# Performance work log

Measured on AMD Instinct MI355X. Metric: run time of the kernel, lower is better.

## Reference

```python
import jax, jax.numpy as jnp
import numpy as np

EPS = 1e-5
NEG_SLOPE = 0.2  # DGL GATConv default leaky_relu slope


def conv1d_same(x, w, b):
    # x: [N, Cin, T], w: [Cout, Cin, K]
    y = jax.lax.conv_general_dilated(x, w, (1,), 'SAME',
                                     dimension_numbers=('NCW', 'OIW', 'NCW'))
    return y + b[None, :, None]


def gated_conv(x, w1, b1, w2, b2, w3, b3):
    # Temporal_Gated_Conv: relu(conv1(x)*sigmoid(conv2(x)) + conv3(x))
    return jax.nn.relu(conv1d_same(x, w1, b1) * jax.nn.sigmoid(conv1d_same(x, w2, b2))
                       + conv1d_same(x, w3, b3))


def bn3(x, g, b):
    # BatchNorm1d on [N, C, T]: stats over (N, T), training mode (batch stats)
    m = jnp.mean(x, (0, 2), keepdims=True)
    v = jnp.var(x, (0, 2), keepdims=True)
    return (x - m) * jax.lax.rsqrt(v + EPS) * g[None, :, None] + b[None, :, None]


def bn2(x, g, b):
    # BatchNorm1d on [N, F]: stats over N
    m = jnp.mean(x, 0, keepdims=True)
    v = jnp.var(x, 0, keepdims=True)
    return (x - m) * jax.lax.rsqrt(v + EPS) * g[None, :] + b[None, :]


def setup_inputs() -> dict:
    key = jax.random.key(0)
    ks = jax.random.split(key, 24)
    N, C, T, H, DEG = 20000, 32, 8, 4, 16
    F = C * T          # GAT in/out feats per head = 256
    E = N * DEG
    s = 0.05
    inp = {
        'X': jax.random.normal(ks[0], (N, C, T), jnp.float32),
        'src': jax.random.randint(ks[1], (E,), 0, N, jnp.int32),
        'dst': jax.random.randint(ks[2], (E,), 0, N, jnp.int32),
        # residual_proj: Conv1d(C->C, k=1)
        'rp_w': jax.random.normal(ks[3], (C, C, 1), jnp.float32) * s,
        'rp_b': jnp.zeros((C,), jnp.float32),
        # gated_conv1: three Conv1d(C->C, k=3)
        'g1_w1': jax.random.normal(ks[4], (C, C, 3), jnp.float32) * s,
        'g1_b1': jnp.zeros((C,), jnp.float32),
        'g1_w2': jax.random.normal(ks[5], (C, C, 3), jnp.float32) * s,
        'g1_b2': jnp.zeros((C,), jnp.float32),
        'g1_w3': jax.random.normal(ks[6], (C, C, 3), jnp.float32) * s,
        'g1_b3': jnp.zeros((C,), jnp.float32),
        'bn0_g': jnp.ones((C,), jnp.float32),
        'bn0_b': jnp.zeros((C,), jnp.float32),
        # GATConv: fc [H*F, F], attn_l/attn_r [H, F], bias [H*F]
        'gat_w': jax.random.normal(ks[7], (H * F, F), jnp.float32) * s,
        'attn_l': jax.random.normal(ks[8], (H, F), jnp.float32) * s,
        'attn_r': jax.random.normal(ks[9], (H, F), jnp.float32) * s,
        'gat_bias': jnp.zeros((H * F,), jnp.float32),
        'bn1_g': jnp.ones((H * F,), jnp.float32),
        'bn1_b': jnp.zeros((H * F,), jnp.float32),
        # gated_conv2: three Conv1d(C*H -> C, k=3)
        'g2_w1': jax.random.normal(ks[10], (C, C * H, 3), jnp.float32) * s,
        'g2_b1': jnp.zeros((C,), jnp.float32),
        'g2_w2': jax.random.normal(ks[11], (C, C * H, 3), jnp.float32) * s,
        'g2_b2': jnp.zeros((C,), jnp.float32),
        'g2_w3': jax.random.normal(ks[12], (C, C * H, 3), jnp.float32) * s,
        'g2_b3': jnp.zeros((C,), jnp.float32),
        'bn2_g': jnp.ones((C,), jnp.float32),
        'bn2_b': jnp.zeros((C,), jnp.float32),
    }
    return inp


def reference(X, src, dst, rp_w, rp_b, g1_w1, g1_b1, g1_w2, g1_b2, g1_w3, g1_b3,
              bn0_g, bn0_b, gat_w, attn_l, attn_r, gat_bias, bn1_g, bn1_b,
              g2_w1, g2_b1, g2_w2, g2_b2, g2_w3, g2_b3, bn2_g, bn2_b):
    N, C, T = X.shape
    H, F = attn_l.shape

    residual = conv1d_same(X, rp_w, rp_b)                      # [N, C, T]
    x = gated_conv(X, g1_w1, g1_b1, g1_w2, g1_b2, g1_w3, g1_b3)
    x = bn3(x, bn0_g, bn0_b)
    x = x.reshape(N, C * T)                                    # row-major flatten == torch .view

    # --- DGL GATConv (feat_drop=attn_drop=0, concat heads, ReLU activation) ---
    h = (x @ gat_w.T).reshape(N, H, F)                         # fc projection
    el = jnp.sum(h * attn_l, -1)                               # [N, H]
    er = jnp.sum(h * attn_r, -1)                               # [N, H]
    e = jax.nn.leaky_relu(el[src] + er[dst], NEG_SLOPE)        # [E, H]
    # segment softmax over incoming edges of each dst node
    m = jax.ops.segment_max(e, dst, num_segments=N)            # [N, H]
    ee = jnp.exp(e - m[dst])
    den = jax.ops.segment_sum(ee, dst, num_segments=N)         # [N, H]
    alpha = ee / den[dst]                                      # [E, H]
    rst = jax.ops.segment_sum(alpha[:, :, None] * h[src], dst, num_segments=N)  # [N, H, F]
    rst = jax.nn.relu(rst + gat_bias.reshape(H, F))

    x = rst.reshape(N, H * F)                                  # concat heads
    x = bn2(x, bn1_g, bn1_b)
    x = x.reshape(N, (H * F) // T, T)                          # [N, C*H, T]
    x = gated_conv(x, g2_w1, g2_b1, g2_w2, g2_b2, g2_w3, g2_b3)
    x = bn3(x, bn2_g, bn2_b)
    x = jax.nn.relu(x + residual)                              # self.last=True, dropout=0
    return x
```

## Files before the change

### kernel.cpp

```cpp
#include <hip/hip_runtime.h>
#include <stdint.h>

#define NN 20000
#define NE 320000

typedef unsigned short us16;
typedef __attribute__((ext_vector_type(8))) short short8;
typedef __attribute__((ext_vector_type(4))) float f32x4;

union U4 { uint4 v; us16 s[8]; unsigned u[4]; };
union U2 { uint2 v; us16 s[4]; };

__device__ __forceinline__ float b2f(us16 u){ return __uint_as_float(((unsigned)u)<<16); }
__device__ __forceinline__ us16 f2b(float f){
  unsigned u = __float_as_uint(f);
  u += 0x7fffu + ((u>>16)&1u);
  return (us16)(u>>16);
}

__device__ __forceinline__ void gll16(const void* g, void* l){
  __builtin_amdgcn_global_load_lds((const __attribute__((address_space(1))) void*)g,
                                   (__attribute__((address_space(3))) void*)l, 16, 0, 0);
}

__global__ __launch_bounds__(256) void k_misc(
    const float* __restrict__ gatw, us16* __restrict__ Wb,
    const float* __restrict__ w1, const float* __restrict__ w2, const float* __restrict__ w3,
    us16* __restrict__ Wt,
    const float* __restrict__ c1w1, const float* __restrict__ c1w2, const float* __restrict__ c1w3,
    const float* __restrict__ rp_w, us16* __restrict__ Wt1,
    const float* __restrict__ attnl, const float* __restrict__ attnr,
    float* __restrict__ wl, float* __restrict__ wr,
    const int* __restrict__ dst, int* __restrict__ counts)
{
  const int b = blockIdx.x, tid = threadIdx.x;
  if(b < 256){
    int i = b*256 + tid;
    float4 v = *(const float4*)(gatw + (size_t)i*4);
    U2 o;
    o.s[0]=f2b(v.x); o.s[1]=f2b(v.y); o.s[2]=f2b(v.z); o.s[3]=f2b(v.w);
    *(uint2*)(Wb + (size_t)i*4) = o.v;
  } else if(b < 400){
    int i = (b-256)*256 + tid;
    int s = i/12288, rem = i%12288;
    int co3 = rem>>7, ci = rem&127;
    const float* w = (co3<32) ? w1 : (co3<64) ? w2 : w3;
    Wt[i] = f2b(w[(co3&31)*384 + ci*3 + s]);
  } else if(b < 448){
    int i = (b-400)*256 + tid;
    int s = i>>12, rem = i&4095;
    int co3 = rem>>5, ci = rem&31;
    float v;
    if(co3 < 96){
      const float* w = (co3<32) ? c1w1 : (co3<64) ? c1w2 : c1w3;
      v = w[(co3&31)*96 + ci*3 + s];
    } else {
      v = (s==1) ? rp_w[(co3-96)*32 + ci] : 0.f;
    }
    Wt1[i] = f2b(v);
  } else if(b < 480){
    int bb = b-448;
    int sel = bb>>4, hd = (bb>>2)&3, fq = bb&3;
    const float* attn = sel ? attnr : attnl;
    int k = tid;
    float s = 0.f;
    int f0 = fq*64;
    #pragma unroll 8
    for(int f=f0; f<f0+64; f++)
      s = fmaf(attn[hd*256+f], gatw[(size_t)(hd*256+f)*256 + k], s);
    atomicAdd(&((sel ? wr : wl)[hd*256+k]), s);
  } else {
    int e = (b-480)*256 + tid;
    if(e < NE) atomicAdd(&counts[dst[e]], 1);
  }
}

__global__ __launch_bounds__(256) void k_gemm1(
    const float* __restrict__ X, const us16* __restrict__ Wt1,
    const float* __restrict__ b1, const float* __restrict__ b2, const float* __restrict__ b3,
    const float* __restrict__ rp_b,
    us16* __restrict__ gc1, us16* __restrict__ resid,
    float* __restrict__ bn0_sum, float* __restrict__ bn0_sq,
    const int* __restrict__ counts, int* __restrict__ offsets, int* __restrict__ cursor)
{
  __shared__ float smemF[5760];
  __shared__ float redS[32], redQ[32];
  __shared__ int wred[4];
  const int tid = threadIdx.x;
  if(blockIdx.x < 1250){
    us16* As = (us16*)smemF;
    us16* Bs = As + 6400;
    if(tid<32){ redS[tid]=0.f; redQ[tid]=0.f; }
    const int node0 = blockIdx.x*16;
    const int lane = tid&63, wv = tid>>6;
    const int mrow = lane&15, kg = (lane>>4)*8;
    for(int idx=tid; idx<1024; idx+=256){
      int n = idx>>6, rem = idx&63, slot = (rem>>5)*9, ci = rem&31;
      As[n*400 + slot*40 + ci] = 0;
    }
    #pragma unroll
    for(int i=0;i<4;i++){
      int idx = i*256 + tid;
      int n = idx>>6, rem = idx&63, ci = rem>>1, tq = rem&1;
      float4 xv = *(const float4*)(X + (size_t)(node0+n)*256 + ci*8 + tq*4);
      us16* p = &As[n*400 + (tq*4+1)*40 + ci];
      p[0]   = f2b(xv.x);
      p[40]  = f2b(xv.y);
      p[80]  = f2b(xv.z);
      p[120] = f2b(xv.w);
    }
    f32x4 acc[2][8] = {};
    for(int s=0; s<3; s++){
      if(s) __syncthreads();
      #pragma unroll
      for(int i=0;i<2;i++){
        int c = i*256 + tid;
        int co = c>>2, cq = c&3;
        *(uint4*)&Bs[co*40 + cq*8] = *(const uint4*)(Wt1 + s*4096 + co*32 + cq*8);
      }
      __syncthreads();
      short8 af[2], bfr[8];
      #pragma unroll
      for(int i=0;i<2;i++){
        int r = wv*32 + i*16 + mrow;
        af[i] = *(const short8*)&As[(r>>3)*400 + ((r&7)+s)*40 + kg];
      }
      #pragma unroll
      for(int j=0;j<8;j++)
        bfr[j] = *(const short8*)&Bs[(j*16 + mrow)*40 + kg];
      #pragma unroll
      for(int i=0;i<2;i++){
        #pragma unroll
        for(int j=0;j<8;j++)
          acc[i][j] = __builtin_amdgcn_mfma_f32_16x16x32_bf16(af[i], bfr[j], acc[i][j], 0, 0, 0);
      }
    }
    __syncthreads();
    us16* Og = (us16*)smemF;
    us16* Or = Og + 4096;
    const int coA = lane&15, coB = coA+16;
    const float b1A=b1[coA], b2A=b2[coA], b3A=b3[coA], brA=rp_b[coA];
    const float b1B=b1[coB], b2B=b2[coB], b3B=b3[coB], brB=rp_b[coB];
    float sA=0.f, qA=0.f, sB=0.f, qB=0.f;
    const int g = lane>>4;
    #pragma unroll
    for(int i=0;i<2;i++){
      int node = wv*4 + i*2 + (g>>1);
      int t0 = (g&1)*4;
      U2 pA, pB, rA2, rB2;
      #pragma unroll
      for(int r=0;r<4;r++){
        float c1 = acc[i][0][r]+b1A, c2 = acc[i][2][r]+b2A, c3 = acc[i][4][r]+b3A;
        float rr = acc[i][6][r]+brA;
        float sg = 1.f/(1.f+__expf(-c2));
        float v = fmaf(c1,sg,c3); v = v>0.f ? v : 0.f;
        sA += v; qA += v*v;
        pA.s[r]=f2b(v); rA2.s[r]=f2b(rr);
        c1 = acc[i][1][r]+b1B; c2 = acc[i][3][r]+b2B; c3 = acc[i][5][r]+b3B;
        rr = acc[i][7][r]+brB;
        sg = 1.f/(1.f+__expf(-c2));
        v = fmaf(c1,sg,c3); v = v>0.f ? v : 0.f;
        sB += v; qB += v*v;
        pB.s[r]=f2b(v); rB2.s[r]=f2b(rr);
      }
      *(uint2*)&Og[node*256 + coA*8 + t0] = pA.v;
      *(uint2*)&Og[node*256 + coB*8 + t0] = pB.v;
      *(uint2*)&Or[node*256 + coA*8 + t0] = rA2.v;
      *(uint2*)&Or[node*256 + coB*8 + t0] = rB2.v;
    }
    sA += __shfl_xor(sA,16,64); sA += __shfl_xor(sA,32,64);
    qA += __shfl_xor(qA,16,64); qA += __shfl_xor(qA,32,64);
    sB += __shfl_xor(sB,16,64); sB += __shfl_xor(sB,32,64);
    qB += __shfl_xor(qB,16,64); qB += __shfl_xor(qB,32,64);
    if(lane < 16){
      atomicAdd(&redS[coA], sA); atomicAdd(&redQ[coA], qA);
      atomicAdd(&redS[coB], sB); atomicAdd(&redQ[coB], qB);
    }
    __syncthreads();
    #pragma unroll
    for(int i=0;i<2;i++){
      int idx = i*256 + tid;
      *(uint4*)(gc1   + (size_t)node0*256 + (size_t)idx*8) = *(const uint4*)&Og[idx*8];
      *(uint4*)(resid + (size_t)node0*256 + (size_t)idx*8) = *(const uint4*)&Or[idx*8];
    }
    if(tid<32)      atomicAdd(&bn0_sum[tid], redS[tid]);
    else if(tid<64) atomicAdd(&bn0_sq[tid-32], redQ[tid-32]);
  } else {
    const int lane = tid&63, wv = tid>>6;
    int running = 0;
    int4 cur;
    {
      int idx = tid*4;
      cur = *(const int4*)(counts + idx);
    }
    for(int t=0; t<20; t++){
      int4 nxt; nxt.x=0; nxt.y=0; nxt.z=0; nxt.w=0;
      if(t < 19){
        int idx = (t+1)*1024 + tid*4;
        if(idx+3 < NN) nxt = *(const int4*)(counts + idx);
        else {
          if(idx   < NN) nxt.x = counts[idx];
          if(idx+1 < NN) nxt.y = counts[idx+1];
          if(idx+2 < NN) nxt.z = counts[idx+2];
          if(idx+3 < NN) nxt.w = counts[idx+3];
        }
      }
      int s = cur.x + cur.y + cur.z + cur.w;
      int incl = s;
      #pragma unroll
      for(int off=1; off<64; off<<=1){
        int v = __shfl_up(incl, off, 64);
        if(lane >= off) incl += v;
      }
      if(lane==63) wred[wv] = incl;
      __syncthreads();
      int woff = 0, btot = 0;
      #pragma unroll
      for(int w2=0; w2<4; w2++){
        int x = wred[w2];
        btot += x;
        if(w2 < wv) woff += x;
      }
      int e0 = running + woff + incl - s;
      int idx = t*1024 + tid*4;
      int4 o; o.x=e0; o.y=e0+cur.x; o.z=o.y+cur.y; o.w=o.z+cur.z;
      if(idx+3 < NN){
        *(int4*)(offsets+idx) = o;
        *(int4*)(cursor+idx)  = o;
      } else {
        if(idx   < NN){ offsets[idx]  =o.x; cursor[idx]  =o.x; }
        if(idx+1 < NN){ offsets[idx+1]=o.y; cursor[idx+1]=o.y; }
        if(idx+2 < NN){ offsets[idx+2]=o.z; cursor[idx+2]=o.z; }
        if(idx+3 < NN){ offsets[idx+3]=o.w; cursor[idx+3]=o.w; }
      }
      running += btot;
      cur = nxt;
      __syncthreads();
    }
    if(tid==0) offsets[NN] = running;
  }
}

__global__ __launch_bounds__(256) void k_eler2(const us16* __restrict__ gc1,
    const float* __restrict__ bn0_sum, const float* __restrict__ bn0_sq,
    const float* __restrict__ bn0g, const float* __restrict__ bn0b,
    const float* __restrict__ wl, const float* __restrict__ wr,
    float* __restrict__ el, float* __restrict__ er)
{
  __shared__ float sa[32], sb[32];
  const int tid = threadIdx.x;
  if(tid<32){
    float m = bn0_sum[tid]*(1.f/160000.f);
    float v = bn0_sq[tid]*(1.f/160000.f) - m*m;
    float a = bn0g[tid]*rsqrtf(v + 1e-5f);
    sa[tid] = a; sb[tid] = bn0b[tid] - m*a;
  }
  __syncthreads();
  const int wv = tid>>6, lane = tid&63;
  const int node = blockIdx.x*4 + wv;
  U2 g; g.v = *(const uint2*)(gc1 + (size_t)node*256 + lane*4);
  const float a = sa[lane>>1], b = sb[lane>>1];
  float xv[4];
  #pragma unroll
  for(int j=0;j<4;j++) xv[j] = fmaf(a, b2f(g.s[j]), b);
  float res[8];
  #pragma unroll
  for(int hd=0; hd<4; hd++){
    float4 lv = *(const float4*)(wl + hd*256 + lane*4);
    float4 rv = *(const float4*)(wr + hd*256 + lane*4);
    res[hd]   = xv[0]*lv.x + xv[1]*lv.y + xv[2]*lv.z + xv[3]*lv.w;
    res[4+hd] = xv[0]*rv.x + xv[1]*rv.y + xv[2]*rv.z + xv[3]*rv.w;
  }
  #pragma unroll
  for(int o=32;o;o>>=1){
    #pragma unroll
    for(int k=0;k<8;k++) res[k] += __shfl_xor(res[k], o, 64);
  }
  if(lane==0){
    #pragma unroll
    for(int hd=0;hd<4;hd++){ el[node*4+hd]=res[hd]; er[node*4+hd]=res[4+hd]; }
  }
}

__global__ __launch_bounds__(256) void k_scatter(const int* __restrict__ src, const int* __restrict__ dst,
    int* __restrict__ cursor, int* __restrict__ esrc,
    const float* __restrict__ el, const float* __restrict__ er,
    float* __restrict__ ew)
{
  int e = blockIdx.x*256 + threadIdx.x;
  if(e < NE){
    int s = src[e], d = dst[e];
    int pos = atomicAdd(&cursor[d], 1);
    esrc[pos] = s;
    float4 lv = *(const float4*)(el + s*4);
    float4 rv = *(const float4*)(er + d*4);
    float4 sc;
    sc.x = lv.x+rv.x; sc.x = sc.x>0.f ? sc.x : 0.2f*sc.x;
    sc.y = lv.y+rv.y; sc.y = sc.y>0.f ? sc.y : 0.2f*sc.y;
    sc.z = lv.z+rv.z; sc.z = sc.z>0.f ? sc.z : 0.2f*sc.z;
    sc.w = lv.w+rv.w; sc.w = sc.w>0.f ? sc.w : 0.2f*sc.w;
    *(float4*)(ew + (size_t)pos*4) = sc;
  }
}

__global__ __launch_bounds__(256) void k_agg2(
    const int* __restrict__ offsets, const int* __restrict__ esrc,
    const float* __restrict__ ew, const us16* __restrict__ gc1,
    const float* __restrict__ bn0_sum, const float* __restrict__ bn0_sq,
    const float* __restrict__ bn0g, const float* __restrict__ bn0b,
    us16* __restrict__ Axg)
{
  const int tid = threadIdx.x;
  const int wv = tid>>6, lane = tid&63;
  const int node = blockIdx.x*4 + wv;
  const int ch = lane>>1;
  float mmn = bn0_sum[ch]*(1.f/160000.f);
  float vvn = bn0_sq[ch]*(1.f/160000.f) - mmn*mmn;
  float sa = bn0g[ch]*rsqrtf(vvn + 1e-5f);
  float sb = bn0b[ch] - mmn*sa;
  const int beg = offsets[node];
  const int deg = offsets[node+1] - beg;
  const int h = lane>>4, i0 = lane&15;
  float m = -3.0e38f;
  for(int i=i0; i<deg; i+=16) m = fmaxf(m, ew[(size_t)(beg+i)*4 + h]);
  m = fmaxf(m, __shfl_xor(m,1,64)); m = fmaxf(m, __shfl_xor(m,2,64));
  m = fmaxf(m, __shfl_xor(m,4,64)); m = fmaxf(m, __shfl_xor(m,8,64));
  float den = 0.f;
  for(int i=i0; i<deg; i+=16) den += __expf(ew[(size_t)(beg+i)*4 + h] - m);
  den += __shfl_xor(den,1,64); den += __shfl_xor(den,2,64);
  den += __shfl_xor(den,4,64); den += __shfl_xor(den,8,64);
  const float m0=__shfl(m,0,64),   m1=__shfl(m,16,64),  m2=__shfl(m,32,64),  m3=__shfl(m,48,64);
  const float d0=__shfl(den,0,64), d1=__shfl(den,16,64),d2=__shfl(den,32,64),d3=__shfl(den,48,64);
  const float v0=d0>0.f?1.f/d0:0.f, v1=d1>0.f?1.f/d1:0.f,
              v2=d2>0.f?1.f/d2:0.f, v3=d3>0.f?1.f/d3:0.f;
  float a0c[4]={},a1c[4]={},a2c[4]={},a3c[4]={};
  #pragma unroll 4
  for(int j=0; j<deg; j++){
    int pos = beg+j;
    float4 w4 = *(const float4*)(ew + (size_t)pos*4);
    int sN = esrc[pos];
    U2 hv; hv.v = *(const uint2*)(gc1 + (size_t)sN*256 + lane*4);
    float e0 = __expf(w4.x-m0)*v0;
    float e1 = __expf(w4.y-m1)*v1;
    float e2 = __expf(w4.z-m2)*v2;
    float e3 = __expf(w4.w-m3)*v3;
    #pragma unroll
    for(int kk=0;kk<4;kk++){
      float x = b2f(hv.s[kk]);
      a0c[kk] = fmaf(e0,x,a0c[kk]);
      a1c[kk] = fmaf(e1,x,a1c[kk]);
      a2c[kk] = fmaf(e2,x,a2c[kk]);
      a3c[kk] = fmaf(e3,x,a3c[kk]);
    }
  }
  const float sbi = sb * ((deg>0)?1.f:0.f);
  U2 o0,o1,o2,o3;
  #pragma unroll
  for(int kk=0;kk<4;kk++){
    o0.s[kk]=f2b(fmaf(sa,a0c[kk],sbi));
    o1.s[kk]=f2b(fmaf(sa,a1c[kk],sbi));
    o2.s[kk]=f2b(fmaf(sa,a2c[kk],sbi));
    o3.s[kk]=f2b(fmaf(sa,a3c[kk],sbi));
  }
  *(uint2*)(Axg + ((size_t)node)*256            + lane*4) = o0.v;
  *(uint2*)(Axg + ((size_t)NN + node)*256       + lane*4) = o1.v;
  *(uint2*)(Axg + ((size_t)2*NN + node)*256     + lane*4) = o2.v;
  *(uint2*)(Axg + ((size_t)3*NN + node)*256     + lane*4) = o3.v;
}

__global__ __launch_bounds__(256) void k_gemm3(const us16* __restrict__ Axg, const us16* __restrict__ Wb,
    const float* __restrict__ gbias, us16* __restrict__ rst,
    float* __restrict__ bn1_sum, float* __restrict__ bn1_sq)
{
  __shared__ us16 sm[17408];
  us16* As = sm;
  us16* Bs = sm + 4096;
  const int tid = threadIdx.x;
  const int row0 = blockIdx.x*128;
  const int cb   = blockIdx.y*128;
  const int hd   = blockIdx.z;
  const us16* A = Axg + (size_t)hd*NN*256;
  const us16* B = Wb  + (size_t)(hd*256 + cb)*256;
  const int lane = tid&63, wv = tid>>6;
  const int wm = wv&1, wn = wv>>1;
  const int mrow = lane&15, g4 = lane>>4;
  const us16* sgA[2]; const us16* sgB[2];
  us16* sdA[2]; us16* sdB[2];
  #pragma unroll
  for(int i=0;i<2;i++){
    int r = (i*4+wv)*16 + (lane>>2);
    int c = (lane&3) ^ (r&3);
    int ga = row0 + r; if(ga >= NN) ga = NN-1;
    sgA[i] = A + (size_t)ga*256 + c*8;
    sgB[i] = B + (size_t)r*256 + c*8;
    sdA[i] = As + (i*4+wv)*512;
    sdB[i] = Bs + (i*4+wv)*512;
  }
  f32x4 acc[4][4] = {};
  for(int k0=0; k0<256; k0+=32){
    if(k0) __syncthreads();
    #pragma unroll
    for(int i=0;i<2;i++){
      gll16(sgA[i] + k0, sdA[i]);
      gll16(sgB[i] + k0, sdB[i]);
    }
    __syncthreads();
    short8 af[4], bfr[4];
    #pragma unroll
    for(int i=0;i<4;i++){
      int r = wm*64 + i*16 + mrow;
      af[i] = *(const short8*)&As[r*32 + ((g4 ^ (r&3))<<3)];
    }
    #pragma unroll
    for(int j=0;j<4;j++){
      int r = wn*64 + j*16 + mrow;
      bfr[j] = *(const short8*)&Bs[r*32 + ((g4 ^ (r&3))<<3)];
    }
    #pragma unroll
    for(int i=0;i<4;i++){
      #pragma unroll
      for(int j=0;j<4;j++)
        acc[i][j] = __builtin_amdgcn_mfma_f32_16x16x32_bf16(af[i], bfr[j], acc[i][j], 0, 0, 0);
    }
  }
  float gb[4];
  #pragma unroll
  for(int j=0;j<4;j++)
    gb[j] = gbias[hd*256 + cb + wn*64 + j*16 + (lane&15)];
  __syncthreads();
  us16* Og = sm;
  float cs[4]={}, cq[4]={};
  #pragma unroll
  for(int i=0;i<4;i++){
    #pragma unroll
    for(int j=0;j<4;j++){
      #pragma unroll
      for(int r=0;r<4;r++){
        int rl = wm*64 + i*16 + (lane>>4)*4 + r;
        float v = acc[i][j][r] + gb[j];
        v = v>0.f ? v : 0.f;
        Og[rl*136 + wn*64 + j*16 + (lane&15)] = f2b(v);
        if(row0 + rl < NN){ cs[j] += v; cq[j] += v*v; }
      }
    }
  }
  #pragma unroll
  for(int j=0;j<4;j++){
    cs[j] += __shfl_xor(cs[j],16,64); cs[j] += __shfl_xor(cs[j],32,64);
    cq[j] += __shfl_xor(cq[j],16,64); cq[j] += __shfl_xor(cq[j],32,64);
  }
  if(lane < 16){
    #pragma unroll
    for(int j=0;j<4;j++){
      int col = hd*256 + cb + wn*64 + j*16 + lane;
      atomicAdd(&bn1_sum[col], cs[j]);
      atomicAdd(&bn1_sq[col],  cq[j]);
    }
  }
  __syncthreads();
  #pragma unroll
  for(int i=0;i<8;i++){
    int idx = i*256 + tid;
    int rowl = idx>>4, cq2 = idx&15;
    int g = row0 + rowl;
    if(g < NN)
      *(uint4*)(rst + (size_t)g*1024 + hd*256 + cb + cq2*8) = *(const uint4*)&Og[rowl*136 + cq2*8];
  }
}

__global__ __launch_bounds__(256) void k_gemm2(
    const us16* __restrict__ rst, const us16* __restrict__ Wt,
    const float* __restrict__ bn1_sum, const float* __restrict__ bn1_sq,
    const float* __restrict__ bn1g, const float* __restrict__ bn1b,
    const float* __restrict__ b1, const float* __restrict__ b2, const float* __restrict__ b3,
    us16* __restrict__ y2, float* __restrict__ bn2_sum, float* __restrict__ bn2_sq)
{
  __shared__ us16 As[11520];
  __shared__ us16 Bs[6912];
  __shared__ float redS[32], redQ[32];
  const int tid = threadIdx.x;
  if(tid<32){ redS[tid]=0.f; redQ[tid]=0.f; }
  const int node0 = blockIdx.x*16;
  const int lane = tid&63, wv = tid>>6;
  const int mrow = lane&15, kg = (lane>>4)*8;
  for(int idx=tid; idx<2048; idx+=256){
    int n = idx>>7, rem = idx&127, slot = (rem>>6)*9, ci = rem&63;
    As[n*720 + slot*72 + ci] = 0;
  }
  f32x4 acc[2][6] = {};
  for(int kc=0; kc<2; kc++){
    float ra[8], rb[8];
    {
      int f0 = (kc*64 + (tid&63))*8;
      float4 s0 = *(const float4*)(bn1_sum + f0), s1 = *(const float4*)(bn1_sum + f0 + 4);
      float4 q0 = *(const float4*)(bn1_sq  + f0), q1 = *(const float4*)(bn1_sq  + f0 + 4);
      float4 g0 = *(const float4*)(bn1g    + f0), g1 = *(const float4*)(bn1g    + f0 + 4);
      float4 h0 = *(const float4*)(bn1b    + f0), h1 = *(const float4*)(bn1b    + f0 + 4);
      const float* sp = (const float*)&s0; const float* qp = (const float*)&q0;
      const float* gp = (const float*)&g0; const float* hp = (const float*)&h0;
      #pragma unroll
      for(int t=0;t<8;t++){
        float sv = (t<4)? sp[t] : ((const float*)&s1)[t-4];
        float qv = (t<4)? qp[t] : ((const float*)&q1)[t-4];
        float gv = (t<4)? gp[t] : ((const float*)&g1)[t-4];
        float hv = (t<4)? hp[t] : ((const float*)&h1)[t-4];
        float m = sv*(1.f/20000.f);
        float v = qv*(1.f/20000.f) - m*m;
        float a = gv*rsqrtf(v + 1e-5f);
        ra[t] = a; rb[t] = hv - m*a;
      }
    }
    if(kc) __syncthreads();
    #pragma unroll
    for(int i=0;i<4;i++){
      int idx = i*256 + tid;
      int n = idx>>6, cil = idx&63;
      int ci = kc*64 + cil;
      U4 in; in.v = *(const uint4*)(rst + (size_t)(node0+n)*1024 + ci*8);
      us16* p = &As[n*720 + 72 + cil];
      #pragma unroll
      for(int t=0;t<8;t++)
        p[t*72] = f2b(fmaf(ra[t], b2f(in.s[t]), rb[t]));
    }
    for(int s=0; s<3; s++){
      if(s) __syncthreads();
      #pragma unroll
      for(int i=0;i<3;i++){
        int chunk = i*256 + tid;
        int brow = chunk>>3, cc = chunk&7;
        *(uint4*)&Bs[brow*72 + cc*8] =
          *(const uint4*)(Wt + s*12288 + brow*128 + kc*64 + cc*8);
      }
      __syncthreads();
      #pragma unroll
      for(int kk=0; kk<64; kk+=32){
        short8 af[2], bfr[6];
        #pragma unroll
        for(int i=0;i<2;i++){
          int r = wv*32 + i*16 + mrow;
          af[i] = *(const short8*)&As[(r>>3)*720 + ((r&7)+s)*72 + kk + kg];
        }
        #pragma unroll
        for(int j=0;j<6;j++)
          bfr[j] = *(const short8*)&Bs[(j*16 + mrow)*72 + kk + kg];
        #pragma unroll
        for(int i=0;i<2;i++){
          #pragma unroll
          for(int j=0;j<6;j++)
            acc[i][j] = __builtin_amdgcn_mfma_f32_16x16x32_bf16(af[i], bfr[j], acc[i][j], 0, 0, 0);
        }
      }
    }
  }
  __syncthreads();
  us16* Og = (us16*)As;
  const int coA = lane&15, coB = coA+16;
  const float b1A=b1[coA], b2A=b2[coA], b3A=b3[coA];
  const float b1B=b1[coB], b2B=b2[coB], b3B=b3[coB];
  float sA=0.f, qA=0.f, sB=0.f, qB=0.f;
  const int g = lane>>4;
  #pragma unroll
  for(int i=0;i<2;i++){
    int node = wv*4 + i*2 + (g>>1);
    int t0 = (g&1)*4;
    U2 pA, pB;
    #pragma unroll
    for(int r=0;r<4;r++){
      float c1 = acc[i][0][r]+b1A, c2 = acc[i][2][r]+b2A, c3 = acc[i][4][r]+b3A;
      float sg = 1.f/(1.f+__expf(-c2));
      float v = fmaf(c1,sg,c3); v = v>0.f ? v : 0.f;
      sA += v; qA += v*v; pA.s[r]=f2b(v);
      c1 = acc[i][1][r]+b1B; c2 = acc[i][3][r]+b2B; c3 = acc[i][5][r]+b3B;
      sg = 1.f/(1.f+__expf(-c2));
      v = fmaf(c1,sg,c3); v = v>0.f ? v : 0.f;
      sB += v; qB += v*v; pB.s[r]=f2b(v);
    }
    *(uint2*)&Og[node*256 + coA*8 + t0] = pA.v;
    *(uint2*)&Og[node*256 + coB*8 + t0] = pB.v;
  }
  sA += __shfl_xor(sA,16,64); sA += __shfl_xor(sA,32,64);
  qA += __shfl_xor(qA,16,64); qA += __shfl_xor(qA,32,64);
  sB += __shfl_xor(sB,16,64); sB += __shfl_xor(sB,32,64);
  qB += __shfl_xor(qB,16,64); qB += __shfl_xor(qB,32,64);
  if(lane < 16){
    atomicAdd(&redS[coA], sA); atomicAdd(&redQ[coA], qA);
    atomicAdd(&redS[coB], sB); atomicAdd(&redQ[coB], qB);
  }
  __syncthreads();
  #pragma unroll
  for(int i=0;i<2;i++){
    int idx = i*256 + tid;
    *(uint4*)(y2 + (size_t)node0*256 + (size_t)idx*8) = *(const uint4*)&Og[idx*8];
  }
  if(tid<32)      atomicAdd(&bn2_sum[tid], redS[tid]);
  else if(tid<64) atomicAdd(&bn2_sq[tid-32], redQ[tid-32]);
}

__global__ __launch_bounds__(256) void k_final(const us16* __restrict__ y2,
    const float* __restrict__ bn2_sum, const float* __restrict__ bn2_sq,
    const float* __restrict__ bn2g, const float* __restrict__ bn2b,
    const us16* __restrict__ resid, float* __restrict__ out)
{
  __shared__ float fa[32], fb[32];
  const int tid = threadIdx.x;
  if(tid<32){
    float m = bn2_sum[tid]*(1.f/160000.f);
    float v = bn2_sq[tid]*(1.f/160000.f) - m*m;
    float a = bn2g[tid]*rsqrtf(v + 1e-5f);
    fa[tid] = a; fb[tid] = bn2b[tid] - m*a;
  }
  __syncthreads();
  size_t base = ((size_t)blockIdx.x*256 + tid)*8;
  int ch = (int)((base>>3)&31);
  float a = fa[ch], b = fb[ch];
  U4 yv, rv;
  yv.v = *(const uint4*)(y2+base);
  rv.v = *(const uint4*)(resid+base);
  float4 o0, o1;
  float vv[8];
  #pragma unroll
  for(int j=0;j<8;j++){
    float v = fmaf(a, b2f(yv.s[j]), b) + b2f(rv.s[j]);
    vv[j] = v>0.f ? v : 0.f;
  }
  o0.x=vv[0]; o0.y=vv[1]; o0.z=vv[2]; o0.w=vv[3];
  o1.x=vv[4]; o1.y=vv[5]; o1.z=vv[6]; o1.w=vv[7];
  *(float4*)(out+base)   = o0;
  *(float4*)(out+base+4) = o1;
}

extern "C" void kernel_launch(void* const* d_in, const int* in_sizes, int n_in,
                              void* d_out, int out_size, void* d_ws, size_t ws_size,
                              hipStream_t stream)
{
  const float* X    = (const float*)d_in[0];
  const int*  src   = (const int*)d_in[1];
  const int*  dst   = (const int*)d_in[2];
  const float* rp_w = (const float*)d_in[3];
  const float* rp_b = (const float*)d_in[4];
  const float* g1w1 = (const float*)d_in[5];
  const float* g1b1 = (const float*)d_in[6];
  const float* g1w2 = (const float*)d_in[7];
  const float* g1b2 = (const float*)d_in[8];
  const float* g1w3 = (const float*)d_in[9];
  const float* g1b3 = (const float*)d_in[10];
  const float* bn0g = (const float*)d_in[11];
  const float* bn0b = (const float*)d_in[12];
  const float* gatw = (const float*)d_in[13];
  const float* attnl= (const float*)d_in[14];
  const float* attnr= (const float*)d_in[15];
  const float* gbias= (const float*)d_in[16];
  const float* bn1g = (const float*)d_in[17];
  const float* bn1b = (const float*)d_in[18];
  const float* g2w1 = (const float*)d_in[19];
  const float* g2b1 = (const float*)d_in[20];
  const float* g2w2 = (const float*)d_in[21];
  const float* g2b2 = (const float*)d_in[22];
  const float* g2w3 = (const float*)d_in[23];
  const float* g2b3 = (const float*)d_in[24];
  const float* bn2g = (const float*)d_in[25];
  const float* bn2b = (const float*)d_in[26];
  float* out = (float*)d_out;
  (void)in_sizes; (void)n_in; (void)out_size; (void)ws_size;

  char* w = (char*)d_ws;
  float* bn0_sum = (float*)w;
  float* bn0_sq  = bn0_sum + 32;
  float* bn1_sum = bn0_sum + 64;
  float* bn1_sq  = bn1_sum + 1024;
  float* bn2_sum = bn1_sq  + 1024;
  float* bn2_sq  = bn2_sum + 32;
  float* wl      = bn2_sq + 32;
  float* wr      = wl + 1024;
  int*   counts  = (int*)(wr + 1024);
  size_t zeroBytes = (size_t)((char*)(counts + NN) - w);
  int*   offsets = counts + NN;
  int*   cursor  = offsets + 20004;
  int*   esrc    = cursor + NN;
  float* el      = (float*)(esrc + NE);
  float* er      = el + NN*4;
  float* ew      = er + NN*4;
  us16*  wb      = (us16*)(ew + (size_t)NE*4);
  us16*  resid   = wb + 262144;
  us16*  gc1     = resid + 5120000;
  us16*  Axg     = gc1   + 5120000;
  us16*  rst     = Axg   + 20480000;
  us16*  Wt      = rst   + 20480000;
  us16*  Wt1     = Wt    + 36864;
  us16*  y2      = gc1;

  hipMemsetAsync(d_ws, 0, zeroBytes, stream);
  k_misc<<<1730, 256, 0, stream>>>(gatw, wb, g2w1, g2w2, g2w3, Wt,
                                   g1w1, g1w2, g1w3, rp_w, Wt1,
                                   attnl, attnr, wl, wr, dst, counts);
  k_gemm1<<<1251, 256, 0, stream>>>(X, Wt1, g1b1, g1b2, g1b3, rp_b,
                                    gc1, resid, bn0_sum, bn0_sq,
                                    counts, offsets, cursor);
  k_eler2<<<5000, 256, 0, stream>>>(gc1, bn0_sum, bn0_sq, bn0g, bn0b, wl, wr, el, er);
  k_scatter<<<1250, 256, 0, stream>>>(src, dst, cursor, esrc, el, er, ew);
  k_agg2<<<5000, 256, 0, stream>>>(offsets, esrc, ew, gc1, bn0_sum, bn0_sq, bn0g, bn0b, Axg);
  k_gemm3<<<dim3(157, 2, 4), 256, 0, stream>>>(Axg, wb, gbias, rst, bn1_sum, bn1_sq);
  k_gemm2<<<1250, 256, 0, stream>>>(rst, Wt, bn1_sum, bn1_sq, bn1g, bn1b,
                                    g2b1, g2b2, g2b3, y2, bn2_sum, bn2_sq);
  k_final<<<2500, 256, 0, stream>>>(y2, bn2_sum, bn2_sq, bn2g, bn2b, resid, out);
}
```

Baseline: 340.8 us.

## Widen gemm3 block to full 256-column head tile with 512 threads

k_gemm3 now uses 512-thread blocks covering all 256 output columns of a head instead of two 128-column blocks, so each A tile row-slab is loaded from global memory once rather than twice. The epilogue is split into two passes through the shared staging buffer, since it only holds 128 columns. This halves redundant A traffic but halves the block count (628 vs 1256), adds extra syncs in the epilogue, and raises per-block resource use.

```diff
diff --git a/kernel.cpp b/kernel.cpp
--- a/kernel.cpp
+++ b/kernel.cpp
@@ -368,7 +368,7 @@
   *(uint2*)(Axg + ((size_t)3*NN + node)*256     + lane*4) = o3.v;
 }
 
-__global__ __launch_bounds__(256) void k_gemm3(const us16* __restrict__ Axg, const us16* __restrict__ Wb,
+__global__ __launch_bounds__(512) void k_gemm3(const us16* __restrict__ Axg, const us16* __restrict__ Wb,
     const float* __restrict__ gbias, us16* __restrict__ rst,
     float* __restrict__ bn1_sum, float* __restrict__ bn1_sq)
 {
@@ -377,33 +377,34 @@
   us16* Bs = sm + 4096;
   const int tid = threadIdx.x;
   const int row0 = blockIdx.x*128;
-  const int cb   = blockIdx.y*128;
-  const int hd   = blockIdx.z;
-  const us16* A = Axg + (size_t)hd*NN*256;
-  const us16* B = Wb  + (size_t)(hd*256 + cb)*256;
+  const int hd   = blockIdx.y;
+  const us16* A  = Axg + (size_t)hd*NN*256;
+  const us16* Bf = Wb  + (size_t)hd*256*256;
   const int lane = tid&63, wv = tid>>6;
   const int wm = wv&1, wn = wv>>1;
   const int mrow = lane&15, g4 = lane>>4;
-  const us16* sgA[2]; const us16* sgB[2];
-  us16* sdA[2]; us16* sdB[2];
-  #pragma unroll
-  for(int i=0;i<2;i++){
-    int r = (i*4+wv)*16 + (lane>>2);
+  const us16* sgA; const us16* sgB[2];
+  us16 *sdA, *sdB[2];
+  {
+    int r = wv*16 + (lane>>2);
     int c = (lane&3) ^ (r&3);
     int ga = row0 + r; if(ga >= NN) ga = NN-1;
-    sgA[i] = A + (size_t)ga*256 + c*8;
-    sgB[i] = B + (size_t)r*256 + c*8;
-    sdA[i] = As + (i*4+wv)*512;
-    sdB[i] = Bs + (i*4+wv)*512;
+    sgA = A + (size_t)ga*256 + c*8;
+    sdA = As + wv*512;
+    #pragma unroll
+    for(int i=0;i<2;i++){
+      int rb = wv*32 + i*16 + (lane>>2);
+      int cbk = (lane&3) ^ (rb&3);
+      sgB[i] = Bf + (size_t)rb*256 + cbk*8;
+      sdB[i] = Bs + wv*1024 + i*512;
+    }
   }
   f32x4 acc[4][4] = {};
   for(int k0=0; k0<256; k0+=32){
     if(k0) __syncthreads();
-    #pragma unroll
-    for(int i=0;i<2;i++){
-      gll16(sgA[i] + k0, sdA[i]);
-      gll16(sgB[i] + k0, sdB[i]);
-    }
+    gll16(sgA + k0, sdA);
+    gll16(sgB[0] + k0, sdB[0]);
+    gll16(sgB[1] + k0, sdB[1]);
     __syncthreads();
     short8 af[4], bfr[4];
     #pragma unroll
@@ -426,45 +427,50 @@
   float gb[4];
   #pragma unroll
   for(int j=0;j<4;j++)
-    gb[j] = gbias[hd*256 + cb + wn*64 + j*16 + (lane&15)];
-  __syncthreads();
+    gb[j] = gbias[hd*256 + wn*64 + j*16 + (lane&15)];
   us16* Og = sm;
-  float cs[4]={}, cq[4]={};
-  #pragma unroll
-  for(int i=0;i<4;i++){
-    #pragma unroll
-    for(int j=0;j<4;j++){
-      #pragma unroll
-      for(int r=0;r<4;r++){
-        int rl = wm*64 + i*16 + (lane>>4)*4 + r;
-        float v = acc[i][j][r] + gb[j];
-        v = v>0.f ? v : 0.f;
-        Og[rl*136 + wn*64 + j*16 + (lane&15)] = f2b(v);
-        if(row0 + rl < NN){ cs[j] += v; cq[j] += v*v; }
-      }
-    }
-  }
-  #pragma unroll
-  for(int j=0;j<4;j++){
-    cs[j] += __shfl_xor(cs[j],16,64); cs[j] += __shfl_xor(cs[j],32,64);
-    cq[j] += __shfl_xor(cq[j],16,64); cq[j] += __shfl_xor(cq[j],32,64);
-  }
-  if(lane < 16){
-    #pragma unroll
-    for(int j=0;j<4;j++){
-      int col = hd*256 + cb + wn*64 + j*16 + lane;
-      atomicAdd(&bn1_sum[col], cs[j]);
-      atomicAdd(&bn1_sq[col],  cq[j]);
-    }
-  }
-  __syncthreads();
-  #pragma unroll
-  for(int i=0;i<8;i++){
-    int idx = i*256 + tid;
-    int rowl = idx>>4, cq2 = idx&15;
-    int g = row0 + rowl;
-    if(g < NN)
-      *(uint4*)(rst + (size_t)g*1024 + hd*256 + cb + cq2*8) = *(const uint4*)&Og[rowl*136 + cq2*8];
+  #pragma unroll
+  for(int p=0; p<2; p++){
+    __syncthreads();
+    if((wn>>1) == p){
+      float cs[4]={}, cq[4]={};
+      #pragma unroll
+      for(int i=0;i<4;i++){
+        #pragma unroll
+        for(int j=0;j<4;j++){
+          #pragma unroll
+          for(int r=0;r<4;r++){
+            int rl = wm*64 + i*16 + (lane>>4)*4 + r;
+            float v = acc[i][j][r] + gb[j];
+            v = v>0.f ? v : 0.f;
+            Og[rl*136 + (wn&1)*64 + j*16 + (lane&15)] = f2b(v);
+            if(row0 + rl < NN){ cs[j] += v; cq[j] += v*v; }
+          }
+        }
+      }
+      #pragma unroll
+      for(int j=0;j<4;j++){
+        cs[j] += __shfl_xor(cs[j],16,64); cs[j] += __shfl_xor(cs[j],32,64);
+        cq[j] += __shfl_xor(cq[j],16,64); cq[j] += __shfl_xor(cq[j],32,64);
+      }
+      if(lane < 16){
+        #pragma unroll
+        for(int j=0;j<4;j++){
+          int col = hd*256 + p*128 + (wn&1)*64 + j*16 + lane;
+          atomicAdd(&bn1_sum[col], cs[j]);
+          atomicAdd(&bn1_sq[col],  cq[j]);
+        }
+      }
+    }
+    __syncthreads();
+    #pragma unroll
+    for(int i=0;i<4;i++){
+      int idx = i*512 + tid;
+      int rowl = idx>>4, cq2 = idx&15;
+      int g = row0 + rowl;
+      if(g < NN)
+        *(uint4*)(rst + (size_t)g*1024 + hd*256 + p*128 + cq2*8) = *(const uint4*)&Og[rowl*136 + cq2*8];
+    }
   }
 }
 
@@ -699,7 +705,7 @@
   k_eler2<<<5000, 256, 0, stream>>>(gc1, bn0_sum, bn0_sq, bn0g, bn0b, wl, wr, el, er);
   k_scatter<<<1250, 256, 0, stream>>>(src, dst, cursor, esrc, el, er, ew);
   k_agg2<<<5000, 256, 0, stream>>>(offsets, esrc, ew, gc1, bn0_sum, bn0_sq, bn0g, bn0b, Axg);
-  k_gemm3<<<dim3(157, 2, 4), 256, 0, stream>>>(Axg, wb, gbias, rst, bn1_sum, bn1_sq);
+  k_gemm3<<<dim3(157, 4), 512, 0, stream>>>(Axg, wb, gbias, rst, bn1_sum, bn1_sq);
   k_gemm2<<<1250, 256, 0, stream>>>(rst, Wt, bn1_sum, bn1_sq, bn1g, bn1b,
                                     g2b1, g2b2, g2b3, y2, bn2_sum, bn2_sq);
   k_final<<<2500, 256, 0, stream>>>(y2, bn2_sum, bn2_sq, bn2g, bn2b, resid, out);
```

New measurement: 348.6 us. 1.02x slower.
